# Kernel optimization log

Measured on AMD Instinct MI355X. Metric: run time of the kernel, lower is better.

Reference implementation:

```python
import jax, jax.numpy as jnp
import numpy as np

EPS = 1e-8
LN_EPS = 1e-5
PSCALE = 10.0
P = 8  # n_points


def _bb_frames(Xn, Xca, Xc):
    # Gram-Schmidt rigid frame from N, CA, C (AlphaFold rigids_from_3_points).
    v1 = Xc - Xca
    v2 = Xn - Xca
    e1 = v1 / jnp.sqrt(jnp.sum(v1 * v1, -1, keepdims=True) + EPS)
    u2 = v2 - e1 * jnp.sum(e1 * v2, -1, keepdims=True)
    e2 = u2 / jnp.sqrt(jnp.sum(u2 * u2, -1, keepdims=True) + EPS)
    e3 = jnp.cross(e1, e2)
    R = jnp.stack([e1, e2, e3], axis=-1)  # [B,N,3,3], columns are basis vectors
    t = Xca / PSCALE                      # scale_translation(1/position_scale)
    return R, t


def _layernorm(x, g, b):
    mu = jnp.mean(x, -1, keepdims=True)
    var = jnp.mean((x - mu) ** 2, -1, keepdims=True)
    return (x - mu) / jnp.sqrt(var + LN_EPS) * g + b


def setup_inputs() -> dict:
    key = jax.random.key(0)
    ks = jax.random.split(key, 24)
    B, N, K, D, H = 8, 512, 32, 128, 128
    msg_in = 2 * D + D + 9 * P  # 456
    s = 0.02
    inp = {
        "h_V": jax.random.normal(ks[0], (B, N, D), jnp.float32),
        "h_E": jax.random.normal(ks[1], (B, N, K, D), jnp.float32),
        "X": jax.random.normal(ks[2], (B, N, 3, 3), jnp.float32),
        "mask_V": jnp.ones((B, N), jnp.float32),
        "mask_attend": jnp.ones((B, N, K), jnp.float32),
        "Wp": jax.random.normal(ks[3], (D, P * 3), jnp.float32) * s,
        "bp": jnp.zeros((P * 3,), jnp.float32),
        "Wm1": jax.random.normal(ks[4], (msg_in, H), jnp.float32) * s,
        "bm1": jnp.zeros((H,), jnp.float32),
        "Wm2": jax.random.normal(ks[5], (H, H), jnp.float32) * s,
        "bm2": jnp.zeros((H,), jnp.float32),
        "Wm3": jax.random.normal(ks[6], (H, H), jnp.float32) * s,
        "bm3": jnp.zeros((H,), jnp.float32),
        "g1": jnp.ones((H,), jnp.float32),
        "be1": jnp.zeros((H,), jnp.float32),
        "Wd1": jax.random.normal(ks[7], (H, 4 * H), jnp.float32) * s,
        "bd1": jnp.zeros((4 * H,), jnp.float32),
        "Wd2": jax.random.normal(ks[8], (4 * H, H), jnp.float32) * s,
        "bd2": jnp.zeros((H,), jnp.float32),
        "g2": jnp.ones((H,), jnp.float32),
        "be2": jnp.zeros((H,), jnp.float32),
        "E_idx": jax.random.randint(ks[9], (B, N, K), 0, N, jnp.int32),
    }
    return inp


def reference(h_V, h_E, X, mask_V, mask_attend,
              Wp, bp, Wm1, bm1, Wm2, bm2, Wm3, bm3, g1, be1,
              Wd1, bd1, Wd2, bd2, g2, be2, E_idx):
    B, N, K = E_idx.shape
    R, t = _bb_frames(X[..., 0, :], X[..., 1, :], X[..., 2, :])
    # local points [B,N,P,3]
    p_local = (h_V @ Wp + bp).reshape(B, N, P, 3)
    # global points: R @ p + t
    p_global = jnp.einsum('bnij,bnpj->bnpi', R, p_local) + t[:, :, None, :]
    bidx = jnp.arange(B)[:, None, None]
    nbr_pg = p_global[bidx, E_idx]  # [B,N,K,P,3]
    nbr_hV = h_V[bidx, E_idx]       # [B,N,K,D]
    # distances in global frame
    diff = p_global[:, :, None] - nbr_pg
    npg_norm = jnp.sqrt(jnp.sum(diff * diff, -1) + EPS)  # [B,N,K,P]
    # neighbor points in local frame: R^T (q - t)
    q = nbr_pg - t[:, :, None, None, :]
    nbr_pl = jnp.einsum('bnij,bnkpi->bnkpj', R, q)       # [B,N,K,P,3]
    npl_norm = jnp.sqrt(jnp.sum(nbr_pl * nbr_pl, -1) + EPS)
    pl_norm = jnp.sqrt(jnp.sum(p_local * p_local, -1) + EPS)  # [B,N,P]

    D = h_V.shape[-1]
    node_expand = jnp.broadcast_to(h_V[:, :, None, :], (B, N, K, D))
    pl_flat = jnp.broadcast_to(p_local[:, :, None], (B, N, K, P, 3)).reshape(B, N, K, P * 3)
    pl_norm_e = jnp.broadcast_to(pl_norm[:, :, None, :], (B, N, K, P))
    msg_in = jnp.concatenate([
        node_expand, h_E, nbr_hV,
        pl_flat, pl_norm_e,
        nbr_pl.reshape(B, N, K, P * 3), npl_norm, npg_norm,
    ], axis=-1)

    # node_message_fn: 3-layer MLP with relu
    m = jax.nn.relu(msg_in @ Wm1 + bm1)
    m = jax.nn.relu(m @ Wm2 + bm2)
    m = m @ Wm3 + bm3
    m = m * mask_attend[..., None]
    node_m = jnp.mean(m, axis=-2)  # [B,N,H]

    h = _layernorm(h_V + node_m, g1, be1)  # dropout = identity (eval)
    dense = jax.nn.relu(h @ Wd1 + bd1) @ Wd2 + bd2
    h = _layernorm(h + dense, g2, be2)
    h = h * mask_V[..., None]
    return h, h_E
```

## Files before the change

### kernel.cpp

```cpp
#include <hip/hip_runtime.h>
#include <hip/hip_bf16.h>

typedef __hip_bfloat16 bf16;
typedef __attribute__((ext_vector_type(8))) short s16x8;
typedef __attribute__((ext_vector_type(4))) float f32x4;

#define DEV __device__ __forceinline__

DEV float us2f(unsigned short u){ return __uint_as_float(((unsigned int)u) << 16); }
DEV unsigned short f2us(float f){
    __hip_bfloat16 h = __float2bfloat16(f);
    unsigned short r; __builtin_memcpy(&r, &h, 2); return r;
}
DEV unsigned pack2(float a, float b){ return (unsigned)f2us(a) | ((unsigned)f2us(b) << 16); }

template<bool F32> DEV float ldf(const void* p, long i){
    if (F32) return reinterpret_cast<const float*>(p)[i];
    return us2f(reinterpret_cast<const unsigned short*>(p)[i]);
}
template<bool F32> DEV unsigned short ld16(const void* p, long i){
    if (F32) return f2us(reinterpret_cast<const float*>(p)[i]);
    return reinterpret_cast<const unsigned short*>(p)[i];
}

union U16x8 { uint4 u; s16x8 v; };

DEV bool is_f32(const void* maskV){
    return reinterpret_cast<const unsigned short*>(maskV)[0] != 0x3F80;
}

template<bool F32>
DEV void wtrans_body(const void* Wm1, const void* Wm2, const void* Wm3,
                     const void* Wp, const void* Wd1, const void* Wd2,
                     unsigned short* wt1, unsigned short* wt2, unsigned short* wt3,
                     unsigned short* wpT, unsigned short* wd1T, unsigned short* wd2T,
                     long t)
{
    if (t < 61440) {
        int k = (int)(t >> 7), h = (int)(t & 127);
        wt1[(long)h*480 + k] = (k < 456) ? ld16<F32>(Wm1, (long)k*128 + h) : (unsigned short)0;
    } else if (t < 77824) {
        long t2 = t - 61440; int k = (int)(t2 >> 7), h = (int)(t2 & 127);
        wt2[(long)h*128 + k] = ld16<F32>(Wm2, (long)k*128 + h);
    } else if (t < 94208) {
        long t2 = t - 77824; int k = (int)(t2 >> 7), h = (int)(t2 & 127);
        wt3[(long)h*128 + k] = ld16<F32>(Wm3, (long)k*128 + h);
    } else if (t < 97280) {
        long t2 = t - 94208; int i = (int)(t2 / 24), j = (int)(t2 % 24);
        wpT[(long)j*128 + i] = ld16<F32>(Wp, (long)i*24 + j);
    } else if (t < 162816) {
        long t2 = t - 97280; int k = (int)(t2 >> 9), n = (int)(t2 & 511);
        wd1T[(long)n*128 + k] = ld16<F32>(Wd1, (long)k*512 + n);
    } else if (t < 228352) {
        long t2 = t - 162816; int k = (int)(t2 >> 7), n = (int)(t2 & 127);
        wd2T[(long)n*512 + k] = ld16<F32>(Wd2, (long)k*128 + n);
    }
}

__global__ __launch_bounds__(256) void wtrans_k(
    const void* __restrict__ Wm1, const void* __restrict__ Wm2, const void* __restrict__ Wm3,
    const void* __restrict__ Wp, const void* __restrict__ Wd1, const void* __restrict__ Wd2,
    unsigned short* __restrict__ wt1, unsigned short* __restrict__ wt2,
    unsigned short* __restrict__ wt3, unsigned short* __restrict__ wpT,
    unsigned short* __restrict__ wd1T, unsigned short* __restrict__ wd2T,
    const void* __restrict__ maskV)
{
    long t = (long)blockIdx.x*256 + threadIdx.x;
    if (is_f32(maskV)) wtrans_body<true >(Wm1,Wm2,Wm3,Wp,Wd1,Wd2,wt1,wt2,wt3,wpT,wd1T,wd2T,t);
    else               wtrans_body<false>(Wm1,Wm2,Wm3,Wp,Wd1,Wd2,wt1,wt2,wt3,wpT,wd1T,wd2T,t);
}

template<bool F32>
DEV void uv_body(const void* hV, const void* bm1, const unsigned short* wt1,
                 float* Uw, float* Vw, int r0, int tid)
{
    const int lane = tid & 63, w = tid >> 6;
    const int lm = lane & 15, quad = lane >> 4;

    s16x8 af[4];
    #pragma unroll
    for (int kc=0; kc<4; ++kc) {
        long src = (long)(r0 + lm)*128 + kc*32 + quad*8;
        U16x8 pk;
        if (F32) {
            const float4* vp = reinterpret_cast<const float4*>(reinterpret_cast<const float*>(hV) + src);
            float4 x = vp[0], y = vp[1];
            pk.u.x = pack2(x.x,x.y); pk.u.y = pack2(x.z,x.w);
            pk.u.z = pack2(y.x,y.y); pk.u.w = pack2(y.z,y.w);
        } else {
            pk.u = *reinterpret_cast<const uint4*>(reinterpret_cast<const unsigned short*>(hV) + src);
        }
        af[kc] = pk.v;
    }

    const int koff = w ? 256 : 0;
    f32x4 acc[8];
    #pragma unroll
    for (int nt=0; nt<8; ++nt) {
        float b0 = w ? 0.f : ldf<F32>(bm1, nt*16 + lm);
        f32x4 iv = {b0,b0,b0,b0};
        acc[nt] = iv;
    }
    #pragma unroll
    for (int kc=0; kc<4; ++kc) {
        #pragma unroll
        for (int nt=0; nt<8; ++nt) {
            s16x8 bf = *reinterpret_cast<const s16x8*>(wt1 + (long)(nt*16 + lm)*480 + koff + kc*32 + quad*8);
            acc[nt] = __builtin_amdgcn_mfma_f32_16x16x32_bf16(af[kc], bf, acc[nt], 0,0,0);
        }
    }
    float* out = w ? Vw : Uw;
    #pragma unroll
    for (int nt=0; nt<8; ++nt)
        #pragma unroll
        for (int r=0; r<4; ++r)
            out[(long)(r0 + quad*4 + r)*128 + nt*16 + lm] = acc[nt][r];
}

__global__ __launch_bounds__(128) void uv_k(
    const void* __restrict__ hV, const void* __restrict__ bm1,
    const unsigned short* __restrict__ wt1,
    float* __restrict__ Uw, float* __restrict__ Vw,
    const void* __restrict__ maskV)
{
    int r0 = blockIdx.x * 16, tid = threadIdx.x;
    if (is_f32(maskV)) uv_body<true >(hV, bm1, wt1, Uw, Vw, r0, tid);
    else               uv_body<false>(hV, bm1, wt1, Uw, Vw, r0, tid);
}

struct PrepSmem { float sX[9], sR[9], st[3], spl[24], hvs[128]; };

template<bool F32>
DEV void prep_body(const void* hV, const void* X, const unsigned short* wpT, const void* bp,
                   float* pg, float* pl, float* pln, float* Rw, float* tw,
                   PrepSmem& s, int n, int tid)
{
    if (tid < 9) s.sX[tid] = ldf<F32>(X, (long)n*9 + tid);
    for (int i = tid; i < 128; i += 64) s.hvs[i] = ldf<F32>(hV, (long)n*128 + i);
    __syncthreads();

    if (tid == 0) {
        float Nx=s.sX[0],Ny=s.sX[1],Nz=s.sX[2];
        float Ax=s.sX[3],Ay=s.sX[4],Az=s.sX[5];
        float Cx=s.sX[6],Cy=s.sX[7],Cz=s.sX[8];
        float v1x=Cx-Ax, v1y=Cy-Ay, v1z=Cz-Az;
        float v2x=Nx-Ax, v2y=Ny-Ay, v2z=Nz-Az;
        float r1 = 1.f/sqrtf(v1x*v1x+v1y*v1y+v1z*v1z + 1e-8f);
        float e1x=v1x*r1, e1y=v1y*r1, e1z=v1z*r1;
        float dp = e1x*v2x+e1y*v2y+e1z*v2z;
        float u2x=v2x-e1x*dp, u2y=v2y-e1y*dp, u2z=v2z-e1z*dp;
        float r2 = 1.f/sqrtf(u2x*u2x+u2y*u2y+u2z*u2z + 1e-8f);
        float e2x=u2x*r2, e2y=u2y*r2, e2z=u2z*r2;
        float e3x = e1y*e2z - e1z*e2y;
        float e3y = e1z*e2x - e1x*e2z;
        float e3z = e1x*e2y - e1y*e2x;
        s.sR[0]=e1x; s.sR[1]=e2x; s.sR[2]=e3x;
        s.sR[3]=e1y; s.sR[4]=e2y; s.sR[5]=e3y;
        s.sR[6]=e1z; s.sR[7]=e2z; s.sR[8]=e3z;
        s.st[0]=Ax*0.1f; s.st[1]=Ay*0.1f; s.st[2]=Az*0.1f;
    }
    if (tid < 24) {
        float acc = ldf<F32>(bp, tid);
        const unsigned short* wr = wpT + (long)tid*128;
        #pragma unroll
        for (int c=0;c<16;c++){
            ushort4 w0 = *reinterpret_cast<const ushort4*>(wr + c*8);
            ushort4 w1 = *reinterpret_cast<const ushort4*>(wr + c*8 + 4);
            acc += s.hvs[c*8+0]*us2f(w0.x) + s.hvs[c*8+1]*us2f(w0.y)
                 + s.hvs[c*8+2]*us2f(w0.z) + s.hvs[c*8+3]*us2f(w0.w)
                 + s.hvs[c*8+4]*us2f(w1.x) + s.hvs[c*8+5]*us2f(w1.y)
                 + s.hvs[c*8+6]*us2f(w1.z) + s.hvs[c*8+7]*us2f(w1.w);
        }
        s.spl[tid] = acc;
    }
    __syncthreads();

    if (tid < 24) {
        pl[n*24+tid] = s.spl[tid];
        int p = tid/3, c = tid - p*3;
        float g = s.sR[c*3+0]*s.spl[p*3+0] + s.sR[c*3+1]*s.spl[p*3+1]
                + s.sR[c*3+2]*s.spl[p*3+2] + s.st[c];
        pg[n*24+tid] = g;
    }
    if (tid < 9) Rw[n*9+tid] = s.sR[tid];
    if (tid < 3) tw[n*3+tid] = s.st[tid];
    if (tid < 8) {
        float a=s.spl[tid*3], b=s.spl[tid*3+1], c=s.spl[tid*3+2];
        pln[n*8+tid] = sqrtf(a*a+b*b+c*c + 1e-8f);
    }
}

__global__ __launch_bounds__(64) void prep_k(
    const void* __restrict__ hV, const void* __restrict__ X,
    const unsigned short* __restrict__ wpT, const void* __restrict__ bp,
    float* __restrict__ pg, float* __restrict__ pl, float* __restrict__ pln,
    float* __restrict__ Rw, float* __restrict__ tw, const void* __restrict__ maskV)
{
    __shared__ PrepSmem s;
    int n = blockIdx.x, tid = threadIdx.x;
    if (is_f32(maskV)) prep_body<true >(hV,X,wpT,bp,pg,pl,pln,Rw,tw,s,n,tid);
    else               prep_body<false>(hV,X,wpT,bp,pg,pl,pln,Rw,tw,s,n,tid);
}

#define ASTRIDE 40
#define MSTRIDE 136

struct __align__(16) Mp1Smem {
    union __align__(16) {
        unsigned short geo[3][64*ASTRIDE];
        unsigned short m[64*MSTRIDE];
    } u;
    int   sj[64];
    float smka[64];
    float spg[2][24], spl[2][24], spln[2][8], sR[2][9], st3[2][3];
};

template<bool F32>
DEV void mpnn1_body(
    const void* hV, const void* hE, const void* maskA,
    const void* bm2, const void* bm3, const int* Eidx,
    const float* pg, const float* pl, const float* pln,
    const float* Rw, const float* tw,
    const unsigned short* wt1, const unsigned short* wt2, const unsigned short* wt3,
    const float* Uw, const float* Vw,
    float* nodemsg, void* outE, Mp1Smem& sm, int n0, int tid)
{
    const int lane = tid & 63, w = tid >> 6;
    const int lm = lane & 15, quad = lane >> 4;

    if (tid < 64) { int l = tid >> 5;
        sm.sj[tid] = (((n0+l) >> 9) << 9) + Eidx[(long)(n0+l)*32 + (tid & 31)];
    } else { int t = tid - 64; int l = t >> 5;
        sm.smka[t] = ldf<F32>(maskA, (long)(n0+l)*32 + (t & 31));
    }
    if (tid < 48)        { sm.spg[tid/24][tid%24] = pg[(n0+tid/24)*24 + tid%24]; }
    else if (tid < 96)   { int t=tid-48; sm.spl[t/24][t%24] = pl[(n0+t/24)*24 + t%24]; }
    else if (tid < 112)  { int t=tid-96; sm.spln[t>>3][t&7]  = pln[(n0+(t>>3))*8 + (t&7)]; }
    if (tid < 18)        { sm.sR[tid/9][tid%9] = Rw[(n0+tid/9)*9 + tid%9]; }
    else if (tid < 24)   { int t=tid-18; sm.st3[t/3][t%3] = tw[(n0+t/3)*3 + t%3]; }
    __syncthreads();

    float vg[4][4][4];
    float ug[2][4];
    #pragma unroll
    for (int mt=0; mt<4; ++mt)
        #pragma unroll
        for (int r=0; r<4; ++r) {
            int j = sm.sj[16*mt + quad*4 + r];
            #pragma unroll
            for (int nt=0; nt<4; ++nt)
                vg[mt][r][nt] = Vw[(long)j*128 + 64*w + nt*16 + lm];
        }
    #pragma unroll
    for (int nd=0; nd<2; ++nd)
        #pragma unroll
        for (int nt=0; nt<4; ++nt)
            ug[nd][nt] = Uw[(long)(n0+nd)*128 + 64*w + nt*16 + lm];

    #pragma unroll
    for (int pass=0; pass<4; ++pass) {
        int v = tid + pass*128;
        int row = v >> 3, p = v & 7, nd = row >> 5;
        int j = sm.sj[row];
        float qx = pg[j*24 + p*3 + 0];
        float qy = pg[j*24 + p*3 + 1];
        float qz = pg[j*24 + p*3 + 2];
        float dx = sm.spg[nd][p*3+0]-qx, dy = sm.spg[nd][p*3+1]-qy, dz = sm.spg[nd][p*3+2]-qz;
        float npg = sqrtf(dx*dx+dy*dy+dz*dz + 1e-8f);
        float ux = qx - sm.st3[nd][0], uy = qy - sm.st3[nd][1], uz = qz - sm.st3[nd][2];
        float l0 = sm.sR[nd][0]*ux + sm.sR[nd][3]*uy + sm.sR[nd][6]*uz;
        float l1 = sm.sR[nd][1]*ux + sm.sR[nd][4]*uy + sm.sR[nd][7]*uz;
        float l2v= sm.sR[nd][2]*ux + sm.sR[nd][5]*uy + sm.sR[nd][8]*uz;
        float npl = sqrtf(l0*l0+l1*l1+l2v*l2v + 1e-8f);
        unsigned short* C0 = sm.u.geo[0];
        unsigned short* C1 = sm.u.geo[1];
        unsigned short* C2 = sm.u.geo[2];
        C0[row*ASTRIDE + p*3+0] = f2us(sm.spl[nd][p*3+0]);
        C0[row*ASTRIDE + p*3+1] = f2us(sm.spl[nd][p*3+1]);
        C0[row*ASTRIDE + p*3+2] = f2us(sm.spl[nd][p*3+2]);
        C0[row*ASTRIDE + 24+p]  = f2us(sm.spln[nd][p]);
        C1[row*ASTRIDE + p*3+0] = f2us(l0);
        C1[row*ASTRIDE + p*3+1] = f2us(l1);
        C1[row*ASTRIDE + p*3+2] = f2us(l2v);
        C1[row*ASTRIDE + 24+p]  = f2us(npl);
        C2[row*ASTRIDE + p]     = f2us(npg);
    }
    for (int z = tid; z < 64*24; z += 128) {
        int row = z / 24, col = 8 + (z % 24);
        sm.u.geo[2][row*ASTRIDE + col] = 0;
    }
    __syncthreads();

    const unsigned short* wr1[4];
    #pragma unroll
    for (int nt=0; nt<4; ++nt) wr1[nt] = wt1 + (long)(64*w + nt*16 + lm)*480 + quad*8;

    f32x4 acc[4][4];
    {
        f32x4 zv = {0.f,0.f,0.f,0.f};
        #pragma unroll
        for (int mt=0; mt<4; ++mt)
            #pragma unroll
            for (int nt=0; nt<4; ++nt) acc[mt][nt] = zv;
    }

    #pragma unroll
    for (int c=0; c<4; ++c) {
        s16x8 av[4];
        #pragma unroll
        for (int mt=0; mt<4; ++mt) {
            int row16 = 16*mt + lm, nd = mt >> 1;
            long src = ((long)(n0+nd)*32 + (row16&31))*128 + c*32 + quad*8;
            U16x8 pk;
            if (F32) {
                const float4* vp = reinterpret_cast<const float4*>(reinterpret_cast<const float*>(hE) + src);
                float4 x = vp[0], y = vp[1];
                if (w == 0) {
                    float4* d = reinterpret_cast<float4*>(reinterpret_cast<float*>(outE) + src);
                    d[0] = x; d[1] = y;
                }
                pk.u.x = pack2(x.x,x.y); pk.u.y = pack2(x.z,x.w);
                pk.u.z = pack2(y.x,y.y); pk.u.w = pack2(y.z,y.w);
            } else {
                pk.u = *reinterpret_cast<const uint4*>(reinterpret_cast<const unsigned short*>(hE) + src);
                if (w == 0)
                    *reinterpret_cast<uint4*>(reinterpret_cast<unsigned short*>(outE) + src) = pk.u;
            }
            av[mt] = pk.v;
        }
        #pragma unroll
        for (int nt=0; nt<4; ++nt) {
            s16x8 bf = *reinterpret_cast<const s16x8*>(wr1[nt] + (long)(c+4)*32);
            #pragma unroll
            for (int mt=0; mt<4; ++mt)
                acc[mt][nt] = __builtin_amdgcn_mfma_f32_16x16x32_bf16(av[mt], bf, acc[mt][nt], 0,0,0);
        }
    }
    #pragma unroll
    for (int c=0; c<3; ++c) {
        s16x8 av[4];
        #pragma unroll
        for (int mt=0; mt<4; ++mt)
            av[mt] = *reinterpret_cast<const s16x8*>(&sm.u.geo[c][(16*mt+lm)*ASTRIDE + quad*8]);
        #pragma unroll
        for (int nt=0; nt<4; ++nt) {
            s16x8 bf = *reinterpret_cast<const s16x8*>(wr1[nt] + (long)(c+12)*32);
            #pragma unroll
            for (int mt=0; mt<4; ++mt)
                acc[mt][nt] = __builtin_amdgcn_mfma_f32_16x16x32_bf16(av[mt], bf, acc[mt][nt], 0,0,0);
        }
    }
    __syncthreads();

    #pragma unroll
    for (int mt=0; mt<4; ++mt)
        #pragma unroll
        for (int nt=0; nt<4; ++nt)
            #pragma unroll
            for (int r=0; r<4; ++r)
                sm.u.m[(16*mt + quad*4 + r)*MSTRIDE + 64*w + nt*16 + lm]
                    = f2us(fmaxf(acc[mt][nt][r] + ug[mt>>1][nt] + vg[mt][r][nt], 0.f));
    __syncthreads();

    #pragma unroll
    for (int nt=0; nt<4; ++nt) {
        float b0 = ldf<F32>(bm2, 64*w + nt*16 + lm);
        f32x4 iv = {b0,b0,b0,b0};
        #pragma unroll
        for (int mt=0; mt<4; ++mt) acc[mt][nt] = iv;
    }
    #pragma unroll
    for (int kc=0; kc<4; ++kc) {
        s16x8 av[4];
        #pragma unroll
        for (int mt=0; mt<4; ++mt)
            av[mt] = *reinterpret_cast<const s16x8*>(&sm.u.m[(16*mt+lm)*MSTRIDE + kc*32 + quad*8]);
        #pragma unroll
        for (int nt=0; nt<4; ++nt) {
            s16x8 bf = *reinterpret_cast<const s16x8*>(&wt2[(long)(64*w + nt*16 + lm)*128 + kc*32 + quad*8]);
            #pragma unroll
            for (int mt=0; mt<4; ++mt)
                acc[mt][nt] = __builtin_amdgcn_mfma_f32_16x16x32_bf16(av[mt], bf, acc[mt][nt], 0,0,0);
        }
    }
    __syncthreads();

    #pragma unroll
    for (int mt=0; mt<4; ++mt)
        #pragma unroll
        for (int nt=0; nt<4; ++nt)
            #pragma unroll
            for (int r=0; r<4; ++r)
                sm.u.m[(16*mt + quad*4 + r)*MSTRIDE + 64*w + nt*16 + lm]
                    = f2us(fmaxf(acc[mt][nt][r], 0.f));
    __syncthreads();

    #pragma unroll
    for (int nt=0; nt<4; ++nt) {
        float b0 = ldf<F32>(bm3, 64*w + nt*16 + lm);
        f32x4 iv = {b0,b0,b0,b0};
        #pragma unroll
        for (int mt=0; mt<4; ++mt) acc[mt][nt] = iv;
    }
    #pragma unroll
    for (int kc=0; kc<4; ++kc) {
        s16x8 av[4];
        #pragma unroll
        for (int mt=0; mt<4; ++mt)
            av[mt] = *reinterpret_cast<const s16x8*>(&sm.u.m[(16*mt+lm)*MSTRIDE + kc*32 + quad*8]);
        #pragma unroll
        for (int nt=0; nt<4; ++nt) {
            s16x8 bf = *reinterpret_cast<const s16x8*>(&wt3[(long)(64*w + nt*16 + lm)*128 + kc*32 + quad*8]);
            #pragma unroll
            for (int mt=0; mt<4; ++mt)
                acc[mt][nt] = __builtin_amdgcn_mfma_f32_16x16x32_bf16(av[mt], bf, acc[mt][nt], 0,0,0);
        }
    }

    #pragma unroll
    for (int nt=0; nt<4; ++nt) {
        float s0 = 0.f, s1 = 0.f;
        #pragma unroll
        for (int r=0; r<4; ++r) {
            s0 += acc[0][nt][r] * sm.smka[     quad*4 + r]
                + acc[1][nt][r] * sm.smka[16 + quad*4 + r];
            s1 += acc[2][nt][r] * sm.smka[32 + quad*4 + r]
                + acc[3][nt][r] * sm.smka[48 + quad*4 + r];
        }
        s0 += __shfl_xor(s0, 16); s0 += __shfl_xor(s0, 32);
        s1 += __shfl_xor(s1, 16); s1 += __shfl_xor(s1, 32);
        if (lane < 16) {
            nodemsg[(long)(n0  )*128 + 64*w + nt*16 + lane] = s0;
            nodemsg[(long)(n0+1)*128 + 64*w + nt*16 + lane] = s1;
        }
    }
}

__global__ __launch_bounds__(128) void mpnn1_k(
    const void* __restrict__ hV, const void* __restrict__ hE,
    const void* __restrict__ maskV, const void* __restrict__ maskA,
    const void* __restrict__ bm2, const void* __restrict__ bm3,
    const int* __restrict__ Eidx,
    const float* __restrict__ pg, const float* __restrict__ pl,
    const float* __restrict__ pln, const float* __restrict__ Rw,
    const float* __restrict__ tw,
    const unsigned short* __restrict__ wt1, const unsigned short* __restrict__ wt2,
    const unsigned short* __restrict__ wt3,
    const float* __restrict__ Uw, const float* __restrict__ Vw,
    float* __restrict__ nodemsg, void* __restrict__ dout)
{
    __shared__ Mp1Smem sm;
    int n0 = blockIdx.x * 2, tid = threadIdx.x;
    if (is_f32(maskV)) {
        void* outE = reinterpret_cast<float*>(dout) + 524288;
        mpnn1_body<true >(hV,hE,maskA,bm2,bm3,Eidx,pg,pl,pln,Rw,tw,wt1,wt2,wt3,Uw,Vw,nodemsg,outE,sm,n0,tid);
    } else {
        void* outE = reinterpret_cast<unsigned short*>(dout) + 524288;
        mpnn1_body<false>(hV,hE,maskA,bm2,bm3,Eidx,pg,pl,pln,Rw,tw,wt1,wt2,wt3,Uw,Vw,nodemsg,outE,sm,n0,tid);
    }
}

#define TSTRIDE 520

struct __align__(16) FfnSmem {
    unsigned short x1[32*MSTRIDE];
    union __align__(16) {
        unsigned short t1[32*TSTRIDE];
        float yf[32*132];
    } u;
};

template<bool F32>
DEV void ffn_body(const void* hV, const void* maskV, const float* nodemsg,
                  const void* g1, const void* be1, const void* bd1, const void* bd2,
                  const void* g2, const void* be2,
                  const unsigned short* wd1T, const unsigned short* wd2T,
                  void* out, FfnSmem& sm, int n0, int tid)
{
    const int lane = tid & 63, w = tid >> 6;
    const int mt = w >> 1, h = w & 1;
    const int lm = lane & 15, quad = lane >> 4;

    {
        const int r = tid >> 3, c0 = (tid & 7) * 16;
        const long nb = (long)(n0 + r)*128;
        float xv[16];
        float s1 = 0.f, s2 = 0.f;
        #pragma unroll
        for (int j=0; j<16; ++j) {
            float v = ldf<F32>(hV, nb + c0 + j) + nodemsg[nb + c0 + j] * (1.f/32.f);
            xv[j] = v; s1 += v; s2 += v*v;
        }
        s1 += __shfl_xor(s1,1); s1 += __shfl_xor(s1,2); s1 += __shfl_xor(s1,4);
        s2 += __shfl_xor(s2,1); s2 += __shfl_xor(s2,2); s2 += __shfl_xor(s2,4);
        float mu = s1 * (1.f/128.f);
        float var = s2 * (1.f/128.f) - mu*mu;
        float rs = 1.f/sqrtf(var + 1e-5f);
        #pragma unroll
        for (int j=0; j<16; ++j) {
            int c = c0 + j;
            sm.x1[r*MSTRIDE + c] = f2us((xv[j]-mu)*rs*ldf<F32>(g1, c) + ldf<F32>(be1, c));
        }
    }
    __syncthreads();

    {
        f32x4 t1a[16];
        #pragma unroll
        for (int nt=0; nt<16; ++nt) {
            float b0 = ldf<F32>(bd1, 256*h + nt*16 + lm);
            f32x4 iv = {b0,b0,b0,b0};
            t1a[nt] = iv;
        }
        #pragma unroll
        for (int kc=0; kc<4; ++kc) {
            s16x8 a = *reinterpret_cast<const s16x8*>(&sm.x1[(16*mt+lm)*MSTRIDE + kc*32 + quad*8]);
            #pragma unroll
            for (int nt=0; nt<16; ++nt) {
                s16x8 bf = *reinterpret_cast<const s16x8*>(&wd1T[(long)(256*h + nt*16 + lm)*128 + kc*32 + quad*8]);
                t1a[nt] = __builtin_amdgcn_mfma_f32_16x16x32_bf16(a, bf, t1a[nt], 0,0,0);
            }
        }
        #pragma unroll
        for (int nt=0; nt<16; ++nt)
            #pragma unroll
            for (int r=0; r<4; ++r)
                sm.u.t1[(16*mt + quad*4 + r)*TSTRIDE + 256*h + nt*16 + lm] = f2us(fmaxf(t1a[nt][r], 0.f));
    }
    __syncthreads();

    f32x4 yacc[4];
    #pragma unroll
    for (int nt=0; nt<4; ++nt) {
        float b0 = ldf<F32>(bd2, 64*h + nt*16 + lm);
        f32x4 iv = {b0,b0,b0,b0};
        yacc[nt] = iv;
    }
    #pragma unroll
    for (int kc=0; kc<16; ++kc) {
        s16x8 a = *reinterpret_cast<const s16x8*>(&sm.u.t1[(16*mt+lm)*TSTRIDE + kc*32 + quad*8]);
        #pragma unroll
        for (int nt=0; nt<4; ++nt) {
            s16x8 bf = *reinterpret_cast<const s16x8*>(&wd2T[(long)(64*h + nt*16 + lm)*512 + kc*32 + quad*8]);
            yacc[nt] = __builtin_amdgcn_mfma_f32_16x16x32_bf16(a, bf, yacc[nt], 0,0,0);
        }
    }
    __syncthreads();

    #pragma unroll
    for (int nt=0; nt<4; ++nt)
        #pragma unroll
        for (int r=0; r<4; ++r) {
            int rr = 16*mt + quad*4 + r, c = 64*h + nt*16 + lm;
            sm.u.yf[rr*132 + c] = yacc[nt][r] + us2f(sm.x1[rr*MSTRIDE + c]);
        }
    __syncthreads();

    {
        const int r = tid >> 3, c0 = (tid & 7) * 16;
        float yv[16];
        float s1 = 0.f, s2 = 0.f;
        #pragma unroll
        for (int j=0; j<16; ++j) {
            float v = sm.u.yf[r*132 + c0 + j];
            yv[j] = v; s1 += v; s2 += v*v;
        }
        s1 += __shfl_xor(s1,1); s1 += __shfl_xor(s1,2); s1 += __shfl_xor(s1,4);
        s2 += __shfl_xor(s2,1); s2 += __shfl_xor(s2,2); s2 += __shfl_xor(s2,4);
        float mu = s1 * (1.f/128.f);
        float var = s2 * (1.f/128.f) - mu*mu;
        float rs = 1.f/sqrtf(var + 1e-5f);
        float mv = ldf<F32>(maskV, n0 + r);
        const long ob = (long)(n0 + r)*128 + c0;
        #pragma unroll
        for (int j=0; j<16; ++j) {
            int c = c0 + j;
            float v = ((yv[j]-mu)*rs*ldf<F32>(g2, c) + ldf<F32>(be2, c)) * mv;
            if (F32) reinterpret_cast<float*>(out)[ob + j] = v;
            else     reinterpret_cast<unsigned short*>(out)[ob + j] = f2us(v);
        }
    }
}

__global__ __launch_bounds__(256) void ffn_k(
    const void* __restrict__ hV, const void* __restrict__ maskV,
    const float* __restrict__ nodemsg,
    const void* __restrict__ g1, const void* __restrict__ be1,
    const void* __restrict__ bd1, const void* __restrict__ bd2,
    const void* __restrict__ g2, const void* __restrict__ be2,
    const unsigned short* __restrict__ wd1T, const unsigned short* __restrict__ wd2T,
    void* __restrict__ out)
{
    __shared__ FfnSmem sm;
    int n0 = blockIdx.x * 32, tid = threadIdx.x;
    if (is_f32(maskV))
        ffn_body<true >(hV,maskV,nodemsg,g1,be1,bd1,bd2,g2,be2,wd1T,wd2T,out,sm,n0,tid);
    else
        ffn_body<false>(hV,maskV,nodemsg,g1,be1,bd1,bd2,g2,be2,wd1T,wd2T,out,sm,n0,tid);
}

extern "C" void kernel_launch(void* const* d_in, const int* in_sizes, int n_in,
                              void* d_out, int out_size, void* d_ws, size_t ws_size,
                              hipStream_t stream)
{
    const void* hV    = d_in[0];
    const void* hE    = d_in[1];
    const void* X     = d_in[2];
    const void* maskV = d_in[3];
    const void* maskA = d_in[4];
    const void* Wp    = d_in[5];
    const void* bp    = d_in[6];
    const void* Wm1   = d_in[7];
    const void* bm1   = d_in[8];
    const void* Wm2   = d_in[9];
    const void* bm2   = d_in[10];
    const void* Wm3   = d_in[11];
    const void* bm3   = d_in[12];
    const void* g1    = d_in[13];
    const void* be1   = d_in[14];
    const void* Wd1   = d_in[15];
    const void* bd1   = d_in[16];
    const void* Wd2   = d_in[17];
    const void* bd2   = d_in[18];
    const void* g2    = d_in[19];
    const void* be2   = d_in[20];
    const int*  Eidx  = (const int*)d_in[21];

    float* ws = (float*)d_ws;
    float* pg  = ws;
    float* pl  = ws + 98304;
    float* pln = ws + 196608;
    float* Rw  = ws + 229376;
    float* tw  = ws + 266240;
    float* nm  = ws + 278528;
    unsigned short* wt1  = (unsigned short*)(ws + 802816);
    unsigned short* wt2  = wt1 + 61440;
    unsigned short* wt3  = wt2 + 16384;
    unsigned short* wpT  = wt3 + 16384;
    unsigned short* wd1T = wpT + 3072;
    unsigned short* wd2T = wd1T + 65536;
    float* Uw = ws + 917504;
    float* Vw = Uw + 524288;

    wtrans_k<<<892, 256, 0, stream>>>(Wm1, Wm2, Wm3, Wp, Wd1, Wd2,
                                      wt1, wt2, wt3, wpT, wd1T, wd2T, maskV);

    uv_k<<<256, 128, 0, stream>>>(hV, bm1, wt1, Uw, Vw, maskV);

    prep_k<<<4096, 64, 0, stream>>>(hV, X, wpT, bp, pg, pl, pln, Rw, tw, maskV);

    mpnn1_k<<<2048, 128, 0, stream>>>(hV, hE, maskV, maskA, bm2, bm3, Eidx,
                                      pg, pl, pln, Rw, tw, wt1, wt2, wt3,
                                      Uw, Vw, nm, d_out);

    ffn_k<<<128, 256, 0, stream>>>(hV, maskV, nm, g1, be1, bd1, bd2, g2, be2,
                                   wd1T, wd2T, d_out);
}
```

Baseline: 269.9 us.

## Merge prep, UV and weight-transpose kernels into one launch; bf16 U/V gather

Folds the weight transpose, U/V projection and per-node frame prep into a single pre-kernel with block-range dispatch, so three launches and their serialization become one. The U/V kernel now reads Wm1 directly through shared-memory staging instead of depending on the transposed copy. U/V are stored as bf16, and the message kernel adds them with coalesced row loads after the MFMA instead of scattered fp32 gathers. FFN uses 16-row blocks to double the grid. The trade-offs are extra bf16 rounding on U/V and more shared-memory work and syncs in the message kernel.

```diff
diff --git a/kernel.cpp b/kernel.cpp
--- a/kernel.cpp
+++ b/kernel.cpp
@@ -29,120 +29,36 @@
     return reinterpret_cast<const unsigned short*>(maskV)[0] != 0x3F80;
 }
 
+struct __align__(16) PreSmem {
+    union __align__(16) {
+        unsigned short lwT[128*40];
+        struct {
+            unsigned short lwp[24*132];
+            float sX[2][9], sR[2][9], st3[2][3], spl[2][24], hvs[2][128];
+        } pr;
+    } u;
+};
+
 template<bool F32>
-DEV void wtrans_body(const void* Wm1, const void* Wm2, const void* Wm3,
-                     const void* Wp, const void* Wd1, const void* Wd2,
-                     unsigned short* wt1, unsigned short* wt2, unsigned short* wt3,
-                     unsigned short* wpT, unsigned short* wd1T, unsigned short* wd2T,
-                     long t)
-{
-    if (t < 61440) {
-        int k = (int)(t >> 7), h = (int)(t & 127);
-        wt1[(long)h*480 + k] = (k < 456) ? ld16<F32>(Wm1, (long)k*128 + h) : (unsigned short)0;
-    } else if (t < 77824) {
-        long t2 = t - 61440; int k = (int)(t2 >> 7), h = (int)(t2 & 127);
-        wt2[(long)h*128 + k] = ld16<F32>(Wm2, (long)k*128 + h);
-    } else if (t < 94208) {
-        long t2 = t - 77824; int k = (int)(t2 >> 7), h = (int)(t2 & 127);
-        wt3[(long)h*128 + k] = ld16<F32>(Wm3, (long)k*128 + h);
-    } else if (t < 97280) {
-        long t2 = t - 94208; int i = (int)(t2 / 24), j = (int)(t2 % 24);
-        wpT[(long)j*128 + i] = ld16<F32>(Wp, (long)i*24 + j);
-    } else if (t < 162816) {
-        long t2 = t - 97280; int k = (int)(t2 >> 9), n = (int)(t2 & 511);
-        wd1T[(long)n*128 + k] = ld16<F32>(Wd1, (long)k*512 + n);
-    } else if (t < 228352) {
-        long t2 = t - 162816; int k = (int)(t2 >> 7), n = (int)(t2 & 127);
-        wd2T[(long)n*512 + k] = ld16<F32>(Wd2, (long)k*128 + n);
-    }
-}
-
-__global__ __launch_bounds__(256) void wtrans_k(
-    const void* __restrict__ Wm1, const void* __restrict__ Wm2, const void* __restrict__ Wm3,
-    const void* __restrict__ Wp, const void* __restrict__ Wd1, const void* __restrict__ Wd2,
-    unsigned short* __restrict__ wt1, unsigned short* __restrict__ wt2,
-    unsigned short* __restrict__ wt3, unsigned short* __restrict__ wpT,
-    unsigned short* __restrict__ wd1T, unsigned short* __restrict__ wd2T,
-    const void* __restrict__ maskV)
-{
-    long t = (long)blockIdx.x*256 + threadIdx.x;
-    if (is_f32(maskV)) wtrans_body<true >(Wm1,Wm2,Wm3,Wp,Wd1,Wd2,wt1,wt2,wt3,wpT,wd1T,wd2T,t);
-    else               wtrans_body<false>(Wm1,Wm2,Wm3,Wp,Wd1,Wd2,wt1,wt2,wt3,wpT,wd1T,wd2T,t);
-}
-
-template<bool F32>
-DEV void uv_body(const void* hV, const void* bm1, const unsigned short* wt1,
-                 float* Uw, float* Vw, int r0, int tid)
-{
-    const int lane = tid & 63, w = tid >> 6;
-    const int lm = lane & 15, quad = lane >> 4;
-
-    s16x8 af[4];
-    #pragma unroll
-    for (int kc=0; kc<4; ++kc) {
-        long src = (long)(r0 + lm)*128 + kc*32 + quad*8;
-        U16x8 pk;
-        if (F32) {
-            const float4* vp = reinterpret_cast<const float4*>(reinterpret_cast<const float*>(hV) + src);
-            float4 x = vp[0], y = vp[1];
-            pk.u.x = pack2(x.x,x.y); pk.u.y = pack2(x.z,x.w);
-            pk.u.z = pack2(y.x,y.y); pk.u.w = pack2(y.z,y.w);
-        } else {
-            pk.u = *reinterpret_cast<const uint4*>(reinterpret_cast<const unsigned short*>(hV) + src);
-        }
-        af[kc] = pk.v;
-    }
-
-    const int koff = w ? 256 : 0;
-    f32x4 acc[8];
-    #pragma unroll
-    for (int nt=0; nt<8; ++nt) {
-        float b0 = w ? 0.f : ldf<F32>(bm1, nt*16 + lm);
-        f32x4 iv = {b0,b0,b0,b0};
-        acc[nt] = iv;
-    }
-    #pragma unroll
-    for (int kc=0; kc<4; ++kc) {
-        #pragma unroll
-        for (int nt=0; nt<8; ++nt) {
-            s16x8 bf = *reinterpret_cast<const s16x8*>(wt1 + (long)(nt*16 + lm)*480 + koff + kc*32 + quad*8);
-            acc[nt] = __builtin_amdgcn_mfma_f32_16x16x32_bf16(af[kc], bf, acc[nt], 0,0,0);
-        }
-    }
-    float* out = w ? Vw : Uw;
-    #pragma unroll
-    for (int nt=0; nt<8; ++nt)
-        #pragma unroll
-        for (int r=0; r<4; ++r)
-            out[(long)(r0 + quad*4 + r)*128 + nt*16 + lm] = acc[nt][r];
-}
-
-__global__ __launch_bounds__(128) void uv_k(
-    const void* __restrict__ hV, const void* __restrict__ bm1,
-    const unsigned short* __restrict__ wt1,
-    float* __restrict__ Uw, float* __restrict__ Vw,
-    const void* __restrict__ maskV)
-{
-    int r0 = blockIdx.x * 16, tid = threadIdx.x;
-    if (is_f32(maskV)) uv_body<true >(hV, bm1, wt1, Uw, Vw, r0, tid);
-    else               uv_body<false>(hV, bm1, wt1, Uw, Vw, r0, tid);
-}
-
-struct PrepSmem { float sX[9], sR[9], st[3], spl[24], hvs[128]; };
-
-template<bool F32>
-DEV void prep_body(const void* hV, const void* X, const unsigned short* wpT, const void* bp,
-                   float* pg, float* pl, float* pln, float* Rw, float* tw,
-                   PrepSmem& s, int n, int tid)
-{
-    if (tid < 9) s.sX[tid] = ldf<F32>(X, (long)n*9 + tid);
-    for (int i = tid; i < 128; i += 64) s.hvs[i] = ldf<F32>(hV, (long)n*128 + i);
-    __syncthreads();
-
-    if (tid == 0) {
-        float Nx=s.sX[0],Ny=s.sX[1],Nz=s.sX[2];
-        float Ax=s.sX[3],Ay=s.sX[4],Az=s.sX[5];
-        float Cx=s.sX[6],Cy=s.sX[7],Cz=s.sX[8];
+DEV void pre_prep(const void* hV, const void* X, const void* Wp, const void* bp,
+                  float* pg, float* pl, float* pln, float* Rw, float* tw,
+                  PreSmem& s, int bid, int tid)
+{
+    auto& pr = s.u.pr;
+    for (int e = tid; e < 3072; e += 128) {
+        int i = e / 24, j = e - i*24;
+        pr.lwp[j*132 + i] = ld16<F32>(Wp, e);
+    }
+    const int wv = tid >> 6, ln = tid & 63;
+    const int n = bid*2 + wv;
+    if (ln < 9) pr.sX[wv][ln] = ldf<F32>(X, (long)n*9 + ln);
+    for (int i = ln; i < 128; i += 64) pr.hvs[wv][i] = ldf<F32>(hV, (long)n*128 + i);
+    __syncthreads();
+
+    if (ln == 0) {
+        float Nx=pr.sX[wv][0],Ny=pr.sX[wv][1],Nz=pr.sX[wv][2];
+        float Ax=pr.sX[wv][3],Ay=pr.sX[wv][4],Az=pr.sX[wv][5];
+        float Cx=pr.sX[wv][6],Cy=pr.sX[wv][7],Cz=pr.sX[wv][8];
         float v1x=Cx-Ax, v1y=Cy-Ay, v1z=Cz-Az;
         float v2x=Nx-Ax, v2y=Ny-Ay, v2z=Nz-Az;
         float r1 = 1.f/sqrtf(v1x*v1x+v1y*v1y+v1z*v1z + 1e-8f);
@@ -154,52 +70,151 @@
         float e3x = e1y*e2z - e1z*e2y;
         float e3y = e1z*e2x - e1x*e2z;
         float e3z = e1x*e2y - e1y*e2x;
-        s.sR[0]=e1x; s.sR[1]=e2x; s.sR[2]=e3x;
-        s.sR[3]=e1y; s.sR[4]=e2y; s.sR[5]=e3y;
-        s.sR[6]=e1z; s.sR[7]=e2z; s.sR[8]=e3z;
-        s.st[0]=Ax*0.1f; s.st[1]=Ay*0.1f; s.st[2]=Az*0.1f;
-    }
-    if (tid < 24) {
-        float acc = ldf<F32>(bp, tid);
-        const unsigned short* wr = wpT + (long)tid*128;
+        pr.sR[wv][0]=e1x; pr.sR[wv][1]=e2x; pr.sR[wv][2]=e3x;
+        pr.sR[wv][3]=e1y; pr.sR[wv][4]=e2y; pr.sR[wv][5]=e3y;
+        pr.sR[wv][6]=e1z; pr.sR[wv][7]=e2z; pr.sR[wv][8]=e3z;
+        pr.st3[wv][0]=Ax*0.1f; pr.st3[wv][1]=Ay*0.1f; pr.st3[wv][2]=Az*0.1f;
+    }
+    if (ln < 24) {
+        float acc = ldf<F32>(bp, ln);
+        const unsigned short* wr = &pr.lwp[ln*132];
         #pragma unroll
         for (int c=0;c<16;c++){
-            ushort4 w0 = *reinterpret_cast<const ushort4*>(wr + c*8);
-            ushort4 w1 = *reinterpret_cast<const ushort4*>(wr + c*8 + 4);
-            acc += s.hvs[c*8+0]*us2f(w0.x) + s.hvs[c*8+1]*us2f(w0.y)
-                 + s.hvs[c*8+2]*us2f(w0.z) + s.hvs[c*8+3]*us2f(w0.w)
-                 + s.hvs[c*8+4]*us2f(w1.x) + s.hvs[c*8+5]*us2f(w1.y)
-                 + s.hvs[c*8+6]*us2f(w1.z) + s.hvs[c*8+7]*us2f(w1.w);
-        }
-        s.spl[tid] = acc;
-    }
-    __syncthreads();
-
-    if (tid < 24) {
-        pl[n*24+tid] = s.spl[tid];
-        int p = tid/3, c = tid - p*3;
-        float g = s.sR[c*3+0]*s.spl[p*3+0] + s.sR[c*3+1]*s.spl[p*3+1]
-                + s.sR[c*3+2]*s.spl[p*3+2] + s.st[c];
-        pg[n*24+tid] = g;
-    }
-    if (tid < 9) Rw[n*9+tid] = s.sR[tid];
-    if (tid < 3) tw[n*3+tid] = s.st[tid];
-    if (tid < 8) {
-        float a=s.spl[tid*3], b=s.spl[tid*3+1], c=s.spl[tid*3+2];
-        pln[n*8+tid] = sqrtf(a*a+b*b+c*c + 1e-8f);
-    }
-}
-
-__global__ __launch_bounds__(64) void prep_k(
+            #pragma unroll
+            for (int k=0;k<8;k++)
+                acc += pr.hvs[wv][c*8+k] * us2f(wr[c*8+k]);
+        }
+        pr.spl[wv][ln] = acc;
+    }
+    __syncthreads();
+
+    if (ln < 24) {
+        pl[n*24+ln] = pr.spl[wv][ln];
+        int p = ln/3, c = ln - p*3;
+        float g = pr.sR[wv][c*3+0]*pr.spl[wv][p*3+0] + pr.sR[wv][c*3+1]*pr.spl[wv][p*3+1]
+                + pr.sR[wv][c*3+2]*pr.spl[wv][p*3+2] + pr.st3[wv][c];
+        pg[n*24+ln] = g;
+    }
+    if (ln < 9) Rw[n*9+ln] = pr.sR[wv][ln];
+    if (ln < 3) tw[n*3+ln] = pr.st3[wv][ln];
+    if (ln < 8) {
+        float a=pr.spl[wv][ln*3], b=pr.spl[wv][ln*3+1], c=pr.spl[wv][ln*3+2];
+        pln[n*8+ln] = sqrtf(a*a+b*b+c*c + 1e-8f);
+    }
+}
+
+template<bool F32>
+DEV void pre_uv(const void* hV, const void* bm1, const void* Wm1,
+                unsigned short* Uw, unsigned short* Vw,
+                PreSmem& s, int r0, int tid)
+{
+    const int lane = tid & 63, w2 = tid >> 6;
+    const int lm = lane & 15, quad = lane >> 4;
+
+    s16x8 af[4];
+    #pragma unroll
+    for (int kc=0; kc<4; ++kc) {
+        long src = (long)(r0 + lm)*128 + kc*32 + quad*8;
+        U16x8 pk;
+        if (F32) {
+            const float4* vp = reinterpret_cast<const float4*>(reinterpret_cast<const float*>(hV) + src);
+            float4 x = vp[0], y = vp[1];
+            pk.u.x = pack2(x.x,x.y); pk.u.y = pack2(x.z,x.w);
+            pk.u.z = pack2(y.x,y.y); pk.u.w = pack2(y.z,y.w);
+        } else {
+            pk.u = *reinterpret_cast<const uint4*>(reinterpret_cast<const unsigned short*>(hV) + src);
+        }
+        af[kc] = pk.v;
+    }
+
+    f32x4 accU[4], accV[4];
+    #pragma unroll
+    for (int nt=0; nt<4; ++nt) {
+        float b0 = ldf<F32>(bm1, 64*w2 + nt*16 + lm);
+        f32x4 iv = {b0,b0,b0,b0};
+        accU[nt] = iv;
+        f32x4 zv = {0.f,0.f,0.f,0.f};
+        accV[nt] = zv;
+    }
+
+    for (int p=0; p<8; ++p) {
+        int k0 = (p<4) ? p*32 : 256 + (p-4)*32;
+        __syncthreads();
+        for (int e = tid; e < 4096; e += 128) {
+            int kk = e >> 7, c = e & 127;
+            s.u.lwT[c*40 + kk] = ld16<F32>(Wm1, (long)k0*128 + e);
+        }
+        __syncthreads();
+        s16x8 a = af[p & 3];
+        #pragma unroll
+        for (int nt=0; nt<4; ++nt) {
+            s16x8 bf = *reinterpret_cast<const s16x8*>(&s.u.lwT[(64*w2 + nt*16 + lm)*40 + quad*8]);
+            if (p < 4) accU[nt] = __builtin_amdgcn_mfma_f32_16x16x32_bf16(a, bf, accU[nt], 0,0,0);
+            else       accV[nt] = __builtin_amdgcn_mfma_f32_16x16x32_bf16(a, bf, accV[nt], 0,0,0);
+        }
+    }
+    #pragma unroll
+    for (int nt=0; nt<4; ++nt)
+        #pragma unroll
+        for (int r=0; r<4; ++r) {
+            long o = (long)(r0 + quad*4 + r)*128 + 64*w2 + nt*16 + lm;
+            Uw[o] = f2us(accU[nt][r]);
+            Vw[o] = f2us(accV[nt][r]);
+        }
+}
+
+template<bool F32>
+DEV void pre_wt(const void* Wm1, const void* Wm2, const void* Wm3,
+                const void* Wd1, const void* Wd2,
+                unsigned short* wt1, unsigned short* wt2, unsigned short* wt3,
+                unsigned short* wd1T, unsigned short* wd2T, long t)
+{
+    if (t < 61440) {
+        int k = (int)(t >> 7), h = (int)(t & 127);
+        wt1[(long)h*480 + k] = (k < 456) ? ld16<F32>(Wm1, (long)k*128 + h) : (unsigned short)0;
+    } else if (t < 77824) {
+        long t2 = t - 61440; int k = (int)(t2 >> 7), h = (int)(t2 & 127);
+        wt2[(long)h*128 + k] = ld16<F32>(Wm2, (long)k*128 + h);
+    } else if (t < 94208) {
+        long t2 = t - 77824; int k = (int)(t2 >> 7), h = (int)(t2 & 127);
+        wt3[(long)h*128 + k] = ld16<F32>(Wm3, (long)k*128 + h);
+    } else if (t < 159744) {
+        long t2 = t - 94208; int k = (int)(t2 >> 9), n = (int)(t2 & 511);
+        wd1T[(long)n*128 + k] = ld16<F32>(Wd1, (long)k*512 + n);
+    } else {
+        long t2 = t - 159744; int k = (int)(t2 >> 7), n = (int)(t2 & 127);
+        wd2T[(long)n*512 + k] = ld16<F32>(Wd2, (long)k*128 + n);
+    }
+}
+
+__global__ __launch_bounds__(128) void pre_k(
     const void* __restrict__ hV, const void* __restrict__ X,
-    const unsigned short* __restrict__ wpT, const void* __restrict__ bp,
+    const void* __restrict__ Wp, const void* __restrict__ bp,
+    const void* __restrict__ Wm1, const void* __restrict__ bm1,
+    const void* __restrict__ Wm2, const void* __restrict__ Wm3,
+    const void* __restrict__ Wd1, const void* __restrict__ Wd2,
     float* __restrict__ pg, float* __restrict__ pl, float* __restrict__ pln,
-    float* __restrict__ Rw, float* __restrict__ tw, const void* __restrict__ maskV)
-{
-    __shared__ PrepSmem s;
-    int n = blockIdx.x, tid = threadIdx.x;
-    if (is_f32(maskV)) prep_body<true >(hV,X,wpT,bp,pg,pl,pln,Rw,tw,s,n,tid);
-    else               prep_body<false>(hV,X,wpT,bp,pg,pl,pln,Rw,tw,s,n,tid);
+    float* __restrict__ Rw, float* __restrict__ tw,
+    unsigned short* __restrict__ Uw, unsigned short* __restrict__ Vw,
+    unsigned short* __restrict__ wt1, unsigned short* __restrict__ wt2,
+    unsigned short* __restrict__ wt3, unsigned short* __restrict__ wd1T,
+    unsigned short* __restrict__ wd2T, const void* __restrict__ maskV)
+{
+    __shared__ PreSmem s;
+    int bid = blockIdx.x, tid = threadIdx.x;
+    bool f32 = is_f32(maskV);
+    if (bid < 2048) {
+        if (f32) pre_prep<true >(hV,X,Wp,bp,pg,pl,pln,Rw,tw,s,bid,tid);
+        else     pre_prep<false>(hV,X,Wp,bp,pg,pl,pln,Rw,tw,s,bid,tid);
+    } else if (bid < 2304) {
+        int r0 = (bid - 2048) * 16;
+        if (f32) pre_uv<true >(hV,bm1,Wm1,Uw,Vw,s,r0,tid);
+        else     pre_uv<false>(hV,bm1,Wm1,Uw,Vw,s,r0,tid);
+    } else {
+        long t = (long)(bid - 2304)*128 + tid;
+        if (f32) pre_wt<true >(Wm1,Wm2,Wm3,Wd1,Wd2,wt1,wt2,wt3,wd1T,wd2T,t);
+        else     pre_wt<false>(Wm1,Wm2,Wm3,Wd1,Wd2,wt1,wt2,wt3,wd1T,wd2T,t);
+    }
 }
 
 #define ASTRIDE 40
@@ -213,6 +228,7 @@
     int   sj[64];
     float smka[64];
     float spg[2][24], spl[2][24], spln[2][8], sR[2][9], st3[2][3];
+    unsigned short sU[2*128];
 };
 
 template<bool F32>
@@ -222,7 +238,7 @@
     const float* pg, const float* pl, const float* pln,
     const float* Rw, const float* tw,
     const unsigned short* wt1, const unsigned short* wt2, const unsigned short* wt3,
-    const float* Uw, const float* Vw,
+    const unsigned short* Uw, const unsigned short* Vw,
     float* nodemsg, void* outE, Mp1Smem& sm, int n0, int tid)
 {
     const int lane = tid & 63, w = tid >> 6;
@@ -238,24 +254,9 @@
     else if (tid < 112)  { int t=tid-96; sm.spln[t>>3][t&7]  = pln[(n0+(t>>3))*8 + (t&7)]; }
     if (tid < 18)        { sm.sR[tid/9][tid%9] = Rw[(n0+tid/9)*9 + tid%9]; }
     else if (tid < 24)   { int t=tid-18; sm.st3[t/3][t%3] = tw[(n0+t/3)*3 + t%3]; }
-    __syncthreads();
-
-    float vg[4][4][4];
-    float ug[2][4];
-    #pragma unroll
-    for (int mt=0; mt<4; ++mt)
-        #pragma unroll
-        for (int r=0; r<4; ++r) {
-            int j = sm.sj[16*mt + quad*4 + r];
-            #pragma unroll
-            for (int nt=0; nt<4; ++nt)
-                vg[mt][r][nt] = Vw[(long)j*128 + 64*w + nt*16 + lm];
-        }
-    #pragma unroll
-    for (int nd=0; nd<2; ++nd)
-        #pragma unroll
-        for (int nt=0; nt<4; ++nt)
-            ug[nd][nt] = Uw[(long)(n0+nd)*128 + 64*w + nt*16 + lm];
+    for (int e = tid; e < 256; e += 128)
+        sm.sU[e] = Uw[(long)(n0 + (e>>7))*128 + (e & 127)];
+    __syncthreads();
 
     #pragma unroll
     for (int pass=0; pass<4; ++pass) {
@@ -359,7 +360,34 @@
             #pragma unroll
             for (int r=0; r<4; ++r)
                 sm.u.m[(16*mt + quad*4 + r)*MSTRIDE + 64*w + nt*16 + lm]
-                    = f2us(fmaxf(acc[mt][nt][r] + ug[mt>>1][nt] + vg[mt][r][nt], 0.f));
+                    = f2us(acc[mt][nt][r]);
+
+    const int row = tid >> 1, ch = tid & 1;
+    const int jv = sm.sj[row];
+    const unsigned short* vrow = Vw + (long)jv*128 + ch*64;
+    uint4 pv[8];
+    #pragma unroll
+    for (int b=0;b<8;++b) pv[b] = *reinterpret_cast<const uint4*>(vrow + b*8);
+    __syncthreads();
+
+    {
+        unsigned short* mrow = &sm.u.m[row*MSTRIDE + ch*64];
+        const unsigned short* urow = &sm.sU[(row>>5)*128 + ch*64];
+        #pragma unroll
+        for (int b=0;b<8;++b) {
+            U16x8 vm; vm.u = *reinterpret_cast<const uint4*>(mrow + b*8);
+            U16x8 vv; vv.u = pv[b];
+            float f[8];
+            #pragma unroll
+            for (int i=0;i<8;++i)
+                f[i] = fmaxf(us2f((unsigned short)vm.v[i]) + us2f((unsigned short)vv.v[i])
+                             + us2f(urow[b*8+i]), 0.f);
+            uint4 o;
+            o.x = pack2(f[0],f[1]); o.y = pack2(f[2],f[3]);
+            o.z = pack2(f[4],f[5]); o.w = pack2(f[6],f[7]);
+            *reinterpret_cast<uint4*>(mrow + b*8) = o;
+        }
+    }
     __syncthreads();
 
     #pragma unroll
@@ -446,7 +474,7 @@
     const float* __restrict__ tw,
     const unsigned short* __restrict__ wt1, const unsigned short* __restrict__ wt2,
     const unsigned short* __restrict__ wt3,
-    const float* __restrict__ Uw, const float* __restrict__ Vw,
+    const unsigned short* __restrict__ Uw, const unsigned short* __restrict__ Vw,
     float* __restrict__ nodemsg, void* __restrict__ dout)
 {
     __shared__ Mp1Smem sm;
@@ -463,10 +491,10 @@
 #define TSTRIDE 520
 
 struct __align__(16) FfnSmem {
-    unsigned short x1[32*MSTRIDE];
+    unsigned short x1[16*MSTRIDE];
     union __align__(16) {
-        unsigned short t1[32*TSTRIDE];
-        float yf[32*132];
+        unsigned short t1[16*TSTRIDE];
+        float yf[16*132];
     } u;
 };
 
@@ -478,26 +506,27 @@
                   void* out, FfnSmem& sm, int n0, int tid)
 {
     const int lane = tid & 63, w = tid >> 6;
-    const int mt = w >> 1, h = w & 1;
     const int lm = lane & 15, quad = lane >> 4;
 
     {
-        const int r = tid >> 3, c0 = (tid & 7) * 16;
+        const int r = tid >> 4, c0 = (tid & 15) * 8;
         const long nb = (long)(n0 + r)*128;
-        float xv[16];
+        float xv[8];
         float s1 = 0.f, s2 = 0.f;
         #pragma unroll
-        for (int j=0; j<16; ++j) {
+        for (int j=0; j<8; ++j) {
             float v = ldf<F32>(hV, nb + c0 + j) + nodemsg[nb + c0 + j] * (1.f/32.f);
             xv[j] = v; s1 += v; s2 += v*v;
         }
-        s1 += __shfl_xor(s1,1); s1 += __shfl_xor(s1,2); s1 += __shfl_xor(s1,4);
-        s2 += __shfl_xor(s2,1); s2 += __shfl_xor(s2,2); s2 += __shfl_xor(s2,4);
+        s1 += __shfl_xor(s1,1); s1 += __shfl_xor(s1,2);
+        s1 += __shfl_xor(s1,4); s1 += __shfl_xor(s1,8);
+        s2 += __shfl_xor(s2,1); s2 += __shfl_xor(s2,2);
+        s2 += __shfl_xor(s2,4); s2 += __shfl_xor(s2,8);
         float mu = s1 * (1.f/128.f);
         float var = s2 * (1.f/128.f) - mu*mu;
         float rs = 1.f/sqrtf(var + 1e-5f);
         #pragma unroll
-        for (int j=0; j<16; ++j) {
+        for (int j=0; j<8; ++j) {
             int c = c0 + j;
             sm.x1[r*MSTRIDE + c] = f2us((xv[j]-mu)*rs*ldf<F32>(g1, c) + ldf<F32>(be1, c));
         }
@@ -505,75 +534,77 @@
     __syncthreads();
 
     {
-        f32x4 t1a[16];
-        #pragma unroll
-        for (int nt=0; nt<16; ++nt) {
-            float b0 = ldf<F32>(bd1, 256*h + nt*16 + lm);
+        f32x4 t1a[8];
+        #pragma unroll
+        for (int nt=0; nt<8; ++nt) {
+            float b0 = ldf<F32>(bd1, 128*w + nt*16 + lm);
             f32x4 iv = {b0,b0,b0,b0};
             t1a[nt] = iv;
         }
         #pragma unroll
         for (int kc=0; kc<4; ++kc) {
-            s16x8 a = *reinterpret_cast<const s16x8*>(&sm.x1[(16*mt+lm)*MSTRIDE + kc*32 + quad*8]);
-            #pragma unroll
-            for (int nt=0; nt<16; ++nt) {
-                s16x8 bf = *reinterpret_cast<const s16x8*>(&wd1T[(long)(256*h + nt*16 + lm)*128 + kc*32 + quad*8]);
+            s16x8 a = *reinterpret_cast<const s16x8*>(&sm.x1[lm*MSTRIDE + kc*32 + quad*8]);
+            #pragma unroll
+            for (int nt=0; nt<8; ++nt) {
+                s16x8 bf = *reinterpret_cast<const s16x8*>(&wd1T[(long)(128*w + nt*16 + lm)*128 + kc*32 + quad*8]);
                 t1a[nt] = __builtin_amdgcn_mfma_f32_16x16x32_bf16(a, bf, t1a[nt], 0,0,0);
             }
         }
         #pragma unroll
-        for (int nt=0; nt<16; ++nt)
+        for (int nt=0; nt<8; ++nt)
             #pragma unroll
             for (int r=0; r<4; ++r)
-                sm.u.t1[(16*mt + quad*4 + r)*TSTRIDE + 256*h + nt*16 + lm] = f2us(fmaxf(t1a[nt][r], 0.f));
-    }
-    __syncthreads();
-
-    f32x4 yacc[4];
-    #pragma unroll
-    for (int nt=0; nt<4; ++nt) {
-        float b0 = ldf<F32>(bd2, 64*h + nt*16 + lm);
+                sm.u.t1[(quad*4 + r)*TSTRIDE + 128*w + nt*16 + lm] = f2us(fmaxf(t1a[nt][r], 0.f));
+    }
+    __syncthreads();
+
+    f32x4 yacc[2];
+    #pragma unroll
+    for (int nt=0; nt<2; ++nt) {
+        float b0 = ldf<F32>(bd2, 32*w + nt*16 + lm);
         f32x4 iv = {b0,b0,b0,b0};
         yacc[nt] = iv;
     }
     #pragma unroll
     for (int kc=0; kc<16; ++kc) {
-        s16x8 a = *reinterpret_cast<const s16x8*>(&sm.u.t1[(16*mt+lm)*TSTRIDE + kc*32 + quad*8]);
-        #pragma unroll
-        for (int nt=0; nt<4; ++nt) {
-            s16x8 bf = *reinterpret_cast<const s16x8*>(&wd2T[(long)(64*h + nt*16 + lm)*512 + kc*32 + quad*8]);
+        s16x8 a = *reinterpret_cast<const s16x8*>(&sm.u.t1[lm*TSTRIDE + kc*32 + quad*8]);
+        #pragma unroll
+        for (int nt=0; nt<2; ++nt) {
+            s16x8 bf = *reinterpret_cast<const s16x8*>(&wd2T[(long)(32*w + nt*16 + lm)*512 + kc*32 + quad*8]);
             yacc[nt] = __builtin_amdgcn_mfma_f32_16x16x32_bf16(a, bf, yacc[nt], 0,0,0);
         }
     }
     __syncthreads();
 
     #pragma unroll
-    for (int nt=0; nt<4; ++nt)
+    for (int nt=0; nt<2; ++nt)
         #pragma unroll
         for (int r=0; r<4; ++r) {
-            int rr = 16*mt + quad*4 + r, c = 64*h + nt*16 + lm;
+            int rr = quad*4 + r, c = 32*w + nt*16 + lm;
             sm.u.yf[rr*132 + c] = yacc[nt][r] + us2f(sm.x1[rr*MSTRIDE + c]);
         }
     __syncthreads();
 
     {
-        const int r = tid >> 3, c0 = (tid & 7) * 16;
-        float yv[16];
+        const int r = tid >> 4, c0 = (tid & 15) * 8;
+        float yv[8];
         float s1 = 0.f, s2 = 0.f;
         #pragma unroll
-        for (int j=0; j<16; ++j) {
+        for (int j=0; j<8; ++j) {
             float v = sm.u.yf[r*132 + c0 + j];
             yv[j] = v; s1 += v; s2 += v*v;
         }
-        s1 += __shfl_xor(s1,1); s1 += __shfl_xor(s1,2); s1 += __shfl_xor(s1,4);
-        s2 += __shfl_xor(s2,1); s2 += __shfl_xor(s2,2); s2 += __shfl_xor(s2,4);
+        s1 += __shfl_xor(s1,1); s1 += __shfl_xor(s1,2);
+        s1 += __shfl_xor(s1,4); s1 += __shfl_xor(s1,8);
+        s2 += __shfl_xor(s2,1); s2 += __shfl_xor(s2,2);
+        s2 += __shfl_xor(s2,4); s2 += __shfl_xor(s2,8);
         float mu = s1 * (1.f/128.f);
         float var = s2 * (1.f/128.f) - mu*mu;
         float rs = 1.f/sqrtf(var + 1e-5f);
         float mv = ldf<F32>(maskV, n0 + r);
         const long ob = (long)(n0 + r)*128 + c0;
         #pragma unroll
-        for (int j=0; j<16; ++j) {
+        for (int j=0; j<8; ++j) {
             int c = c0 + j;
             float v = ((yv[j]-mu)*rs*ldf<F32>(g2, c) + ldf<F32>(be2, c)) * mv;
             if (F32) reinterpret_cast<float*>(out)[ob + j] = v;
@@ -592,7 +623,7 @@
     void* __restrict__ out)
 {
     __shared__ FfnSmem sm;
-    int n0 = blockIdx.x * 32, tid = threadIdx.x;
+    int n0 = blockIdx.x * 16, tid = threadIdx.x;
     if (is_f32(maskV))
         ffn_body<true >(hV,maskV,nodemsg,g1,be1,bd1,bd2,g2,be2,wd1T,wd2T,out,sm,n0,tid);
     else
@@ -636,23 +667,19 @@
     unsigned short* wt1  = (unsigned short*)(ws + 802816);
     unsigned short* wt2  = wt1 + 61440;
     unsigned short* wt3  = wt2 + 16384;
-    unsigned short* wpT  = wt3 + 16384;
-    unsigned short* wd1T = wpT + 3072;
+    unsigned short* wd1T = wt3 + 16384;
     unsigned short* wd2T = wd1T + 65536;
-    float* Uw = ws + 917504;
-    float* Vw = Uw + 524288;
-
-    wtrans_k<<<892, 256, 0, stream>>>(Wm1, Wm2, Wm3, Wp, Wd1, Wd2,
-                                      wt1, wt2, wt3, wpT, wd1T, wd2T, maskV);
-
-    uv_k<<<256, 128, 0, stream>>>(hV, bm1, wt1, Uw, Vw, maskV);
-
-    prep_k<<<4096, 64, 0, stream>>>(hV, X, wpT, bp, pg, pl, pln, Rw, tw, maskV);
+    unsigned short* Uw   = wd2T + 65536;
+    unsigned short* Vw   = Uw + 524288;
+
+    pre_k<<<4064, 128, 0, stream>>>(hV, X, Wp, bp, Wm1, bm1, Wm2, Wm3, Wd1, Wd2,
+                                    pg, pl, pln, Rw, tw, Uw, Vw,
+                                    wt1, wt2, wt3, wd1T, wd2T, maskV);
 
     mpnn1_k<<<2048, 128, 0, stream>>>(hV, hE, maskV, maskA, bm2, bm3, Eidx,
                                       pg, pl, pln, Rw, tw, wt1, wt2, wt3,
                                       Uw, Vw, nm, d_out);
 
-    ffn_k<<<128, 256, 0, stream>>>(hV, maskV, nm, g1, be1, bd1, bd2, g2, be2,
+    ffn_k<<<256, 256, 0, stream>>>(hV, maskV, nm, g1, be1, bd1, bd2, g2, be2,
                                    wd1T, wd2T, d_out);
 }
```

After: 245.0 us. -9.2%, faster.
